# Optimization experiments

Hardware: AMD Instinct MI355X
Metric: run time of the kernel (lower is better)

## Reference

```python
import jax, jax.numpy as jnp
import numpy as np

C = 256; HEADS = 8; LEVELS = 4; POINTS = 4; D = C // HEADS
SPATIAL = np.array([[96, 96], [48, 48], [24, 24], [12, 12]], dtype=np.int32)  # (H, W) per level
AREAS = SPATIAL[:, 0] * SPATIAL[:, 1]
HW = int(AREAS.sum())  # 12240
LSI = np.concatenate([[0], np.cumsum(AREAS)[:-1]]).astype(np.int32)
N = 1; Q = HW


def setup_inputs() -> dict:
    key = jax.random.key(0)
    ks = jax.random.split(key, 12)
    s = 0.02
    return {
        "query": jax.random.normal(ks[0], (N, Q, C), jnp.float32),
        "reference_points": jax.random.uniform(ks[1], (N, Q, LEVELS, 2), jnp.float32),
        "input_flatten": jax.random.normal(ks[2], (N, HW, C), jnp.float32),
        "input_spatial_shapes": jnp.asarray(SPATIAL),
        "input_level_start_index": jnp.asarray(LSI),
        "W_off": jax.random.normal(ks[3], (C, HEADS * LEVELS * POINTS * 2), jnp.float32) * s,
        "b_off": jax.random.normal(ks[4], (HEADS * LEVELS * POINTS * 2,), jnp.float32) * s,
        "W_attn": jax.random.normal(ks[5], (C, HEADS * LEVELS * POINTS), jnp.float32) * s,
        "b_attn": jax.random.normal(ks[6], (HEADS * LEVELS * POINTS,), jnp.float32) * s,
        "W_val": jax.random.normal(ks[7], (C, C), jnp.float32) * (1.0 / np.sqrt(C)),
        "b_val": jax.random.normal(ks[8], (C,), jnp.float32) * s,
        "W_out": jax.random.normal(ks[9], (C, C), jnp.float32) * (1.0 / np.sqrt(C)),
        "b_out": jax.random.normal(ks[10], (C,), jnp.float32) * s,
    }


def _ms_deform_attn(query, reference_points, input_flatten, sp, lsi,
                    W_off, b_off, W_attn, b_attn, W_val, b_val, W_out, b_out):
    n, q, c = query.shape
    hw = input_flatten.shape[1]
    # value projection -> [N, Hd, HW, D]
    value = (input_flatten @ W_val + b_val).reshape(n, hw, HEADS, D).transpose(0, 2, 1, 3)
    # sampling offsets [N,Q,Hd,L,P,2]
    off = (query @ W_off + b_off).reshape(n, q, HEADS, LEVELS, POINTS, 2)
    # attention weights softmaxed over L*P (done inside the fused CUDA kernel)
    attn = jax.nn.softmax((query @ W_attn + b_attn).reshape(n, q, HEADS, LEVELS * POINTS), axis=-1)
    attn = attn.reshape(n, q, HEADS, LEVELS, POINTS)
    # normalized sampling locations (reference_points last dim == 2 branch)
    norm = jnp.stack([sp[:, 1], sp[:, 0]], -1).astype(query.dtype)  # (W, H) per level
    loc = reference_points[:, :, None, :, None, :] + off / norm[None, None, None, :, None, :]
    Hl = sp[:, 0][None, None, None, :, None]
    Wl = sp[:, 1][None, None, None, :, None]
    start = lsi[None, None, None, :, None]
    # grid_sample-style (align_corners=False) pixel coordinates
    x = loc[..., 0] * Wl - 0.5
    y = loc[..., 1] * Hl - 0.5
    x0 = jnp.floor(x); y0 = jnp.floor(y)
    lx = x - x0; ly = y - y0
    x0i = x0.astype(jnp.int32); y0i = y0.astype(jnp.int32)

    def gather(yi, xi):
        valid = (xi >= 0) & (xi < Wl) & (yi >= 0) & (yi < Hl)
        idx = jnp.where(valid, start + yi * Wl + xi, 0)  # [N,Q,Hd,L,P]
        idx_t = idx.transpose(0, 2, 1, 3, 4).reshape(n, HEADS, q * LEVELS * POINTS, 1)
        g = jnp.take_along_axis(value, idx_t, axis=2)  # [N,Hd,Q*L*P,D]
        g = g.reshape(n, HEADS, q, LEVELS, POINTS, D)
        return g * valid.transpose(0, 2, 1, 3, 4)[..., None]

    def w(a):
        return a.transpose(0, 2, 1, 3, 4)[..., None]  # [N,Hd,Q,L,P,1]

    sampled = (gather(y0i, x0i) * w((1 - ly) * (1 - lx))
               + gather(y0i, x0i + 1) * w((1 - ly) * lx)
               + gather(y0i + 1, x0i) * w(ly * (1 - lx))
               + gather(y0i + 1, x0i + 1) * w(ly * lx))  # [N,Hd,Q,L,P,D]
    out = jnp.einsum('nhqlpd,nqhlp->nqhd', sampled, attn).reshape(n, q, c)
    return out @ W_out + b_out


def reference(query, reference_points, input_flatten, input_spatial_shapes, input_level_start_index,
              W_off, b_off, W_attn, b_attn, W_val, b_val, W_out, b_out):
    return _ms_deform_attn(query, reference_points, input_flatten,
                           input_spatial_shapes, input_level_start_index,
                           W_off, b_off, W_attn, b_attn, W_val, b_val, W_out, b_out)
```

## Files before the change

### kernel.cpp

```cpp
#include <hip/hip_runtime.h>

#define QTOT 12240
#define KD   256

typedef float f32x4 __attribute__((ext_vector_type(4)));
typedef short s16x8 __attribute__((ext_vector_type(8)));
typedef unsigned short ushort_t;

__device__ __forceinline__ unsigned short f2b(float x) {
    union { float f; unsigned u; } c; c.f = x;
    unsigned r = c.u + 0x7fffu + ((c.u >> 16) & 1u);
    return (unsigned short)(r >> 16);
}
__device__ __forceinline__ int a_off(int row, int kb) { return row * 512 + (kb ^ ((row & 7) << 4)); }
__device__ __forceinline__ int b_off(int n,   int kb) { return n * 128 + (kb ^ ((n & 7) << 4)); }

__global__ __launch_bounds__(256) void prep(
    const float* __restrict__ W_val, const float* __restrict__ W_off,
    const float* __restrict__ W_attn, const float* __restrict__ W_out,
    const float* __restrict__ b_off, const float* __restrict__ b_attn,
    ushort_t* __restrict__ WvT, ushort_t* __restrict__ WcT,
    ushort_t* __restrict__ WoT, float* __restrict__ bcomb)
{
    int id = blockIdx.x * 256 + threadIdx.x;
    if (id < 65536) { int n = id >> 8, k = id & 255; WvT[id] = f2b(W_val[k * 256 + n]); }
    else if (id < 163840) {
        int t = id - 65536; int n = t >> 8, k = t & 255;
        float v = (n < 256) ? W_off[k * 256 + n] : W_attn[k * 128 + (n - 256)];
        WcT[t] = f2b(v);
    } else if (id < 229376) {
        int t = id - 163840; int n = t >> 8, k = t & 255;
        WoT[t] = f2b(W_out[k * 256 + n]);
    } else if (id < 229760) {
        int t = id - 229376; bcomb[t] = (t < 256) ? b_off[t] : b_attn[t - 256];
    }
}

template<int NF>
__device__ __forceinline__ void stageB(const ushort_t* __restrict__ WT, int k0, char* Bs) {
    const int tid = threadIdx.x;
#pragma unroll
    for (int e = 0; e < NF * 2; ++e) {
        int u = e * 256 + tid;
        int n = u >> 3, j = u & 7, js = j ^ (n & 7);
        s16x8 v = *(const s16x8*)(WT + (size_t)n * KD + k0 + js * 8);
        *(s16x8*)(Bs + n * 128 + j * 16) = v;
    }
}

template<int NF>
__device__ __forceinline__ void mm_full(const ushort_t* __restrict__ WT,
                                        char* As, char* Bs, f32x4 (&acc)[2][NF])
{
    const int tid = threadIdx.x, lane = tid & 63, wc = tid >> 6;
    const int lr = lane & 15, g8 = (lane >> 4) * 8;
    for (int k0 = 0; k0 < KD; k0 += 64) {
        __syncthreads();
#pragma unroll
        for (int kk = 0; kk < 2; ++kk) {
            const int kbB = (kk * 32 + g8) * 2;
            const int kbA = (k0 + kk * 32 + g8) * 2;
            s16x8 af0 = *(const s16x8*)(As + a_off(lr, kbA));
            s16x8 af1 = *(const s16x8*)(As + a_off(16 + lr, kbA));
#pragma unroll
            for (int n = 0; n < NF; ++n) {
                s16x8 bf = *(const s16x8*)(Bs + b_off(wc * NF * 16 + n * 16 + lr, kbB));
                acc[0][n] = __builtin_amdgcn_mfma_f32_16x16x32_bf16(af0, bf, acc[0][n], 0, 0, 0);
                acc[1][n] = __builtin_amdgcn_mfma_f32_16x16x32_bf16(af1, bf, acc[1][n], 0, 0, 0);
            }
        }
        __syncthreads();
        if (k0 < 192) stageB<NF>(WT, k0 + 64, Bs);
    }
}

__global__ __launch_bounds__(256) void gemm1(
    const float* __restrict__ inflat, const float* __restrict__ query,
    const ushort_t* __restrict__ WvT, const ushort_t* __restrict__ WcT,
    const float* __restrict__ b_val, const float* __restrict__ bcomb,
    ushort_t* __restrict__ projb, ushort_t* __restrict__ offb,
    float* __restrict__ logitf)
{
    __shared__ char smem[16384 + 49152];
    char* As = smem; char* Bs = smem + 16384;
    const int b = blockIdx.x;
    const bool isval = b < 383;
    const int bm = (isval ? b : b - 383) * 32;
    const float* A = isval ? inflat : query;

    {
        const int row = threadIdx.x >> 3, c0 = (threadIdx.x & 7) * 32;
        const int grow = bm + row;
        float4 f[8];
        if (grow < QTOT) {
            const float4* s = (const float4*)(A + (size_t)grow * KD + c0);
#pragma unroll
            for (int i = 0; i < 8; ++i) f[i] = s[i];
        } else {
#pragma unroll
            for (int i = 0; i < 8; ++i) f[i] = make_float4(0.f, 0.f, 0.f, 0.f);
        }
#pragma unroll
        for (int i = 0; i < 4; ++i) {
            s16x8 v;
            v[0] = f2b(f[2*i].x);   v[1] = f2b(f[2*i].y);
            v[2] = f2b(f[2*i].z);   v[3] = f2b(f[2*i].w);
            v[4] = f2b(f[2*i+1].x); v[5] = f2b(f[2*i+1].y);
            v[6] = f2b(f[2*i+1].z); v[7] = f2b(f[2*i+1].w);
            *(s16x8*)(As + a_off(row, (c0 + i * 8) * 2)) = v;
        }
    }

    const int lane = threadIdx.x & 63, wc = threadIdx.x >> 6;
    const int lr = lane & 15, rg = (lane >> 4) * 4;

    if (isval) {
        f32x4 acc[2][4];
#pragma unroll
        for (int m = 0; m < 2; ++m)
#pragma unroll
            for (int n = 0; n < 4; ++n) acc[m][n] = (f32x4)0.f;
        stageB<4>(WvT, 0, Bs);
        mm_full<4>(WvT, As, Bs, acc);
#pragma unroll
        for (int n = 0; n < 4; ++n) {
            const int col = wc * 64 + n * 16 + lr;
            const float bb = b_val[col];
#pragma unroll
            for (int m = 0; m < 2; ++m)
#pragma unroll
                for (int rr = 0; rr < 4; ++rr) {
                    const int row = bm + m * 16 + rg + rr;
                    if (row < QTOT) projb[(size_t)row * 256 + col] = f2b(acc[m][n][rr] + bb);
                }
        }
    } else {
        f32x4 acc[2][6];
#pragma unroll
        for (int m = 0; m < 2; ++m)
#pragma unroll
            for (int n = 0; n < 6; ++n) acc[m][n] = (f32x4)0.f;
        stageB<6>(WcT, 0, Bs);
        mm_full<6>(WcT, As, Bs, acc);
#pragma unroll
        for (int n = 0; n < 6; ++n) {
            const int col = wc * 96 + n * 16 + lr;
            const float bb = bcomb[col];
#pragma unroll
            for (int m = 0; m < 2; ++m)
#pragma unroll
                for (int rr = 0; rr < 4; ++rr) {
                    const int row = bm + m * 16 + rg + rr;
                    if (row >= QTOT) continue;
                    const float v = acc[m][n][rr] + bb;
                    if (col < 256) offb[(size_t)row * 256 + col] = f2b(v);
                    else           logitf[(size_t)row * 128 + col - 256] = v;
                }
        }
    }
}

__global__ __launch_bounds__(256) void sample4(
    const float* __restrict__ rp, const ushort_t* __restrict__ offb,
    const float* __restrict__ logitf, const ushort_t* __restrict__ projb,
    const int* __restrict__ sp, const int* __restrict__ lsi,
    ushort_t* __restrict__ outpre)
{
    const int bid = blockIdx.x;
    const int qpair = (bid & 7) * 765 + (bid >> 3);
    const int tid = threadIdx.x;
    const int qi = tid >> 7;
    const int q = qpair * 2 + qi;

    __shared__ int   s_idx[256][4];
    __shared__ float s_w[256][4];

    {
        const int t = tid & 127;
        const int l = (t >> 2) & 3;
        float logit = logitf[(size_t)q * 128 + t];
        float mx = logit;
#pragma unroll
        for (int d = 1; d < 16; d <<= 1) mx = fmaxf(mx, __shfl_xor(mx, d));
        float e = __expf(logit - mx);
        float s = e;
#pragma unroll
        for (int d = 1; d < 16; d <<= 1) s += __shfl_xor(s, d);
        const float aw = e / s;

        const unsigned opk = *(const unsigned*)&offb[(size_t)q * 256 + t * 2];
        const float ox = __uint_as_float(opk << 16);
        const float oy = __uint_as_float(opk & 0xffff0000u);

        const int Hl = sp[l * 2], Wl = sp[l * 2 + 1], st = lsi[l];
        const float rx = rp[((size_t)q * 4 + l) * 2 + 0];
        const float ry = rp[((size_t)q * 4 + l) * 2 + 1];

        const float x = rx * (float)Wl + ox - 0.5f;
        const float y = ry * (float)Hl + oy - 0.5f;
        const float xf = floorf(x), yf = floorf(y);
        const int x0 = (int)xf, y0 = (int)yf;
        const float lx = x - xf, ly = y - yf;

        const bool vx0 = (x0 >= 0) && (x0 < Wl);
        const bool vx1 = (x0 + 1 >= 0) && (x0 + 1 < Wl);
        const bool vy0 = (y0 >= 0) && (y0 < Hl);
        const bool vy1 = (y0 + 1 >= 0) && (y0 + 1 < Hl);

        s_w[tid][0] = (vx0 && vy0) ? aw * (1.f - ly) * (1.f - lx) : 0.f;
        s_w[tid][1] = (vx1 && vy0) ? aw * (1.f - ly) * lx         : 0.f;
        s_w[tid][2] = (vx0 && vy1) ? aw * ly * (1.f - lx)         : 0.f;
        s_w[tid][3] = (vx1 && vy1) ? aw * ly * lx                 : 0.f;
        s_idx[tid][0] = (vx0 && vy0) ? (st + y0 * Wl + x0) * 512           : 0;
        s_idx[tid][1] = (vx1 && vy0) ? (st + y0 * Wl + x0 + 1) * 512       : 0;
        s_idx[tid][2] = (vx0 && vy1) ? (st + (y0 + 1) * Wl + x0) * 512     : 0;
        s_idx[tid][3] = (vx1 && vy1) ? (st + (y0 + 1) * Wl + x0 + 1) * 512 : 0;
    }
    __syncthreads();

    const int tt = tid & 127;
    const int h = tt >> 4, qtr = (tt >> 2) & 3, c8 = tt & 3;
    const char* basec = (const char*)projb + (h * 32 + c8 * 8) * 2;

    float a0 = 0, a1 = 0, a2 = 0, a3 = 0, a4 = 0, a5 = 0, a6 = 0, a7 = 0;
#pragma unroll
    for (int p = 0; p < 4; ++p) {
        const int slot = qi * 128 + h * 16 + qtr * 4 + p;
        const int4   id4 = *(const int4*)s_idx[slot];
        const float4 w4  = *(const float4*)s_w[slot];
#pragma unroll
        for (int c = 0; c < 4; ++c) {
            const int   id = (c == 0) ? id4.x : (c == 1) ? id4.y : (c == 2) ? id4.z : id4.w;
            const float w  = (c == 0) ? w4.x  : (c == 1) ? w4.y  : (c == 2) ? w4.z  : w4.w;
            const uint4 v = *(const uint4*)(basec + id);
            a0 += w * __uint_as_float(v.x << 16);
            a1 += w * __uint_as_float(v.x & 0xffff0000u);
            a2 += w * __uint_as_float(v.y << 16);
            a3 += w * __uint_as_float(v.y & 0xffff0000u);
            a4 += w * __uint_as_float(v.z << 16);
            a5 += w * __uint_as_float(v.z & 0xffff0000u);
            a6 += w * __uint_as_float(v.w << 16);
            a7 += w * __uint_as_float(v.w & 0xffff0000u);
        }
    }
    a0 += __shfl_xor(a0, 4); a1 += __shfl_xor(a1, 4);
    a2 += __shfl_xor(a2, 4); a3 += __shfl_xor(a3, 4);
    a4 += __shfl_xor(a4, 4); a5 += __shfl_xor(a5, 4);
    a6 += __shfl_xor(a6, 4); a7 += __shfl_xor(a7, 4);
    a0 += __shfl_xor(a0, 8); a1 += __shfl_xor(a1, 8);
    a2 += __shfl_xor(a2, 8); a3 += __shfl_xor(a3, 8);
    a4 += __shfl_xor(a4, 8); a5 += __shfl_xor(a5, 8);
    a6 += __shfl_xor(a6, 8); a7 += __shfl_xor(a7, 8);

    if (qtr == 0) {
        uint4 o;
        o.x = (unsigned)f2b(a0) | ((unsigned)f2b(a1) << 16);
        o.y = (unsigned)f2b(a2) | ((unsigned)f2b(a3) << 16);
        o.z = (unsigned)f2b(a4) | ((unsigned)f2b(a5) << 16);
        o.w = (unsigned)f2b(a6) | ((unsigned)f2b(a7) << 16);
        *(uint4*)&outpre[(size_t)q * 256 + h * 32 + c8 * 8] = o;
    }
}

__global__ __launch_bounds__(256) void gemm_o(
    const ushort_t* __restrict__ Ab, const ushort_t* __restrict__ WoT,
    const float* __restrict__ b_out, float* __restrict__ out)
{
    __shared__ char smem[8192 + 32768];
    char* As = smem; char* Bs = smem + 8192;
    const int bm = blockIdx.x * 16;

    {
        const int row = threadIdx.x >> 4, cu = (threadIdx.x & 15) * 16;
        const s16x8* s = (const s16x8*)(Ab + (size_t)(bm + row) * KD + cu);
        s16x8 v0 = s[0], v1 = s[1];
        *(s16x8*)(As + a_off(row, cu * 2))      = v0;
        *(s16x8*)(As + a_off(row, cu * 2 + 16)) = v1;
    }

    f32x4 acc[4];
#pragma unroll
    for (int n = 0; n < 4; ++n) acc[n] = (f32x4)0.f;
    stageB<4>(WoT, 0, Bs);

    const int tid = threadIdx.x, lane = tid & 63, wc = tid >> 6;
    const int lr = lane & 15, g8 = (lane >> 4) * 8;
    for (int k0 = 0; k0 < KD; k0 += 64) {
        __syncthreads();
#pragma unroll
        for (int kk = 0; kk < 2; ++kk) {
            const int kbB = (kk * 32 + g8) * 2;
            const int kbA = (k0 + kk * 32 + g8) * 2;
            s16x8 af = *(const s16x8*)(As + a_off(lr, kbA));
#pragma unroll
            for (int n = 0; n < 4; ++n) {
                s16x8 bf = *(const s16x8*)(Bs + b_off(wc * 64 + n * 16 + lr, kbB));
                acc[n] = __builtin_amdgcn_mfma_f32_16x16x32_bf16(af, bf, acc[n], 0, 0, 0);
            }
        }
        __syncthreads();
        if (k0 < 192) stageB<4>(WoT, k0 + 64, Bs);
    }

    const int rg = (lane >> 4) * 4;
#pragma unroll
    for (int n = 0; n < 4; ++n) {
        const int col = wc * 64 + n * 16 + lr;
        const float bb = b_out[col];
#pragma unroll
        for (int rr = 0; rr < 4; ++rr) {
            const int row = bm + rg + rr;
            out[(size_t)row * 256 + col] = acc[n][rr] + bb;
        }
    }
}

extern "C" void kernel_launch(void* const* d_in, const int* in_sizes, int n_in,
                              void* d_out, int out_size, void* d_ws, size_t ws_size,
                              hipStream_t stream) {
    const float* query  = (const float*)d_in[0];
    const float* rp     = (const float*)d_in[1];
    const float* inflat = (const float*)d_in[2];
    const int*   sp     = (const int*)d_in[3];
    const int*   lsi    = (const int*)d_in[4];
    const float* W_off  = (const float*)d_in[5];
    const float* b_off  = (const float*)d_in[6];
    const float* W_attn = (const float*)d_in[7];
    const float* b_attn = (const float*)d_in[8];
    const float* W_val  = (const float*)d_in[9];
    const float* b_val  = (const float*)d_in[10];
    const float* W_out  = (const float*)d_in[11];
    const float* b_out  = (const float*)d_in[12];
    float* out = (float*)d_out;

    char* ws = (char*)d_ws;
    ushort_t* projb  = (ushort_t*)ws; ws += (size_t)QTOT * 256 * 2;
    ushort_t* offb   = (ushort_t*)ws; ws += (size_t)QTOT * 256 * 2;
    float*    logitf = (float*)ws;    ws += (size_t)QTOT * 128 * 4;
    ushort_t* outpre = (ushort_t*)ws; ws += (size_t)QTOT * 256 * 2;
    ushort_t* WvT    = (ushort_t*)ws; ws += 65536 * 2;
    ushort_t* WcT    = (ushort_t*)ws; ws += 98304 * 2;
    ushort_t* WoT    = (ushort_t*)ws; ws += 65536 * 2;
    float*    bcomb  = (float*)ws;    ws += 384 * 4;

    dim3 blk(256);

    prep<<<dim3(898), blk, 0, stream>>>(W_val, W_off, W_attn, W_out, b_off, b_attn,
                                        WvT, WcT, WoT, bcomb);

    gemm1<<<dim3(766), blk, 0, stream>>>(inflat, query, WvT, WcT, b_val, bcomb,
                                         projb, offb, logitf);

    sample4<<<dim3(6120), blk, 0, stream>>>(rp, offb, logitf, projb, sp, lsi, outpre);

    gemm_o<<<dim3(765), blk, 0, stream>>>(outpre, WoT, b_out, out);
}
```

Measured before the change: 70.23 us.

## Retile projection GEMMs into 64x64 output tiles with full-K shared staging

Both GEMM kernels move from narrow row tiles (32 or 16 rows) covering every output column to 64x64 output tiles, with the full K=256 slab of A and B staged into LDS once and a single barrier. The grid is enlarged and block indices are swizzled across 8 groups so more blocks can run concurrently. The intent is to remove the per-K-chunk barrier and staging loop and to raise parallelism. The cost is that the fp32 A rows are reloaded and reconverted once per column tile, which adds A-side global traffic, and the larger LDS footprint per block may reduce occupancy.

```diff
diff --git a/kernel.cpp b/kernel.cpp
--- a/kernel.cpp
+++ b/kernel.cpp
@@ -12,8 +12,7 @@
     unsigned r = c.u + 0x7fffu + ((c.u >> 16) & 1u);
     return (unsigned short)(r >> 16);
 }
-__device__ __forceinline__ int a_off(int row, int kb) { return row * 512 + (kb ^ ((row & 7) << 4)); }
-__device__ __forceinline__ int b_off(int n,   int kb) { return n * 128 + (kb ^ ((n & 7) << 4)); }
+__device__ __forceinline__ int swz(int row, int kb) { return row * 512 + (kb ^ ((row & 7) << 4)); }
 
 __global__ __launch_bounds__(256) void prep(
     const float* __restrict__ W_val, const float* __restrict__ W_off,
@@ -36,41 +35,30 @@
     }
 }
 
-template<int NF>
-__device__ __forceinline__ void stageB(const ushort_t* __restrict__ WT, int k0, char* Bs) {
-    const int tid = threadIdx.x;
-#pragma unroll
-    for (int e = 0; e < NF * 2; ++e) {
-        int u = e * 256 + tid;
-        int n = u >> 3, j = u & 7, js = j ^ (n & 7);
-        s16x8 v = *(const s16x8*)(WT + (size_t)n * KD + k0 + js * 8);
-        *(s16x8*)(Bs + n * 128 + j * 16) = v;
-    }
-}
-
-template<int NF>
-__device__ __forceinline__ void mm_full(const ushort_t* __restrict__ WT,
-                                        char* As, char* Bs, f32x4 (&acc)[2][NF])
-{
-    const int tid = threadIdx.x, lane = tid & 63, wc = tid >> 6;
+__device__ __forceinline__ void stageB_full(const ushort_t* __restrict__ WT, int bn, char* Bs) {
+    const int t = threadIdx.x;
+    const int n = t >> 2, c0 = (t & 3) * 64;
+    const ushort_t* src = WT + (size_t)(bn + n) * KD + c0;
+#pragma unroll
+    for (int j = 0; j < 8; ++j)
+        *(s16x8*)(Bs + swz(n, (c0 + j * 8) * 2)) = *(const s16x8*)(src + j * 8);
+}
+
+__device__ __forceinline__ void mm64(char* As, char* Bs, f32x4 (&acc)[2][2]) {
+    const int tid = threadIdx.x, lane = tid & 63, wave = tid >> 6;
+    const int wr = wave >> 1, wc = wave & 1;
     const int lr = lane & 15, g8 = (lane >> 4) * 8;
-    for (int k0 = 0; k0 < KD; k0 += 64) {
-        __syncthreads();
-#pragma unroll
-        for (int kk = 0; kk < 2; ++kk) {
-            const int kbB = (kk * 32 + g8) * 2;
-            const int kbA = (k0 + kk * 32 + g8) * 2;
-            s16x8 af0 = *(const s16x8*)(As + a_off(lr, kbA));
-            s16x8 af1 = *(const s16x8*)(As + a_off(16 + lr, kbA));
-#pragma unroll
-            for (int n = 0; n < NF; ++n) {
-                s16x8 bf = *(const s16x8*)(Bs + b_off(wc * NF * 16 + n * 16 + lr, kbB));
-                acc[0][n] = __builtin_amdgcn_mfma_f32_16x16x32_bf16(af0, bf, acc[0][n], 0, 0, 0);
-                acc[1][n] = __builtin_amdgcn_mfma_f32_16x16x32_bf16(af1, bf, acc[1][n], 0, 0, 0);
-            }
-        }
-        __syncthreads();
-        if (k0 < 192) stageB<NF>(WT, k0 + 64, Bs);
+#pragma unroll
+    for (int kc = 0; kc < 8; ++kc) {
+        const int kb = (kc * 32 + g8) * 2;
+        s16x8 a0 = *(const s16x8*)(As + swz(wr * 32 + lr,      kb));
+        s16x8 a1 = *(const s16x8*)(As + swz(wr * 32 + 16 + lr, kb));
+        s16x8 b0 = *(const s16x8*)(Bs + swz(wc * 32 + lr,      kb));
+        s16x8 b1 = *(const s16x8*)(Bs + swz(wc * 32 + 16 + lr, kb));
+        acc[0][0] = __builtin_amdgcn_mfma_f32_16x16x32_bf16(a0, b0, acc[0][0], 0, 0, 0);
+        acc[0][1] = __builtin_amdgcn_mfma_f32_16x16x32_bf16(a0, b1, acc[0][1], 0, 0, 0);
+        acc[1][0] = __builtin_amdgcn_mfma_f32_16x16x32_bf16(a1, b0, acc[1][0], 0, 0, 0);
+        acc[1][1] = __builtin_amdgcn_mfma_f32_16x16x32_bf16(a1, b1, acc[1][1], 0, 0, 0);
     }
 }
 
@@ -81,82 +69,124 @@
     ushort_t* __restrict__ projb, ushort_t* __restrict__ offb,
     float* __restrict__ logitf)
 {
-    __shared__ char smem[16384 + 49152];
-    char* As = smem; char* Bs = smem + 16384;
-    const int b = blockIdx.x;
-    const bool isval = b < 383;
-    const int bm = (isval ? b : b - 383) * 32;
-    const float* A = isval ? inflat : query;
+    __shared__ char As[32768];
+    __shared__ char Bs[32768];
+    const int bid = blockIdx.x;
+    const int linear = (bid & 7) * 240 + (bid >> 3);
+    const int mt = linear / 10, nt = linear - mt * 10;
+    const int bm = mt * 64;
+    const bool isval = nt < 4;
+    const int bnc = isval ? nt * 64 : (nt - 4) * 64;
+
+    if (isval) stageB_full(WvT, bnc, Bs);
+    else       stageB_full(WcT, bnc, Bs);
 
     {
-        const int row = threadIdx.x >> 3, c0 = (threadIdx.x & 7) * 32;
+        const int t = threadIdx.x;
+        const int row = t >> 2, c0 = (t & 3) * 64;
         const int grow = bm + row;
-        float4 f[8];
+        const float* A = isval ? inflat : query;
+        float4 f[16];
         if (grow < QTOT) {
             const float4* s = (const float4*)(A + (size_t)grow * KD + c0);
 #pragma unroll
-            for (int i = 0; i < 8; ++i) f[i] = s[i];
+            for (int i = 0; i < 16; ++i) f[i] = s[i];
         } else {
 #pragma unroll
-            for (int i = 0; i < 8; ++i) f[i] = make_float4(0.f, 0.f, 0.f, 0.f);
+            for (int i = 0; i < 16; ++i) f[i] = make_float4(0.f, 0.f, 0.f, 0.f);
         }
 #pragma unroll
-        for (int i = 0; i < 4; ++i) {
+        for (int j = 0; j < 8; ++j) {
             s16x8 v;
-            v[0] = f2b(f[2*i].x);   v[1] = f2b(f[2*i].y);
-            v[2] = f2b(f[2*i].z);   v[3] = f2b(f[2*i].w);
-            v[4] = f2b(f[2*i+1].x); v[5] = f2b(f[2*i+1].y);
-            v[6] = f2b(f[2*i+1].z); v[7] = f2b(f[2*i+1].w);
-            *(s16x8*)(As + a_off(row, (c0 + i * 8) * 2)) = v;
+            v[0] = f2b(f[2*j].x);   v[1] = f2b(f[2*j].y);
+            v[2] = f2b(f[2*j].z);   v[3] = f2b(f[2*j].w);
+            v[4] = f2b(f[2*j+1].x); v[5] = f2b(f[2*j+1].y);
+            v[6] = f2b(f[2*j+1].z); v[7] = f2b(f[2*j+1].w);
+            *(s16x8*)(As + swz(row, (c0 + j * 8) * 2)) = v;
         }
     }
-
-    const int lane = threadIdx.x & 63, wc = threadIdx.x >> 6;
+    __syncthreads();
+
+    f32x4 acc[2][2];
+#pragma unroll
+    for (int m = 0; m < 2; ++m)
+#pragma unroll
+        for (int n = 0; n < 2; ++n) acc[m][n] = (f32x4)0.f;
+    mm64(As, Bs, acc);
+
+    const int lane = threadIdx.x & 63, wave = threadIdx.x >> 6;
+    const int wr = wave >> 1, wc = wave & 1;
     const int lr = lane & 15, rg = (lane >> 4) * 4;
-
-    if (isval) {
-        f32x4 acc[2][4];
+#pragma unroll
+    for (int n = 0; n < 2; ++n) {
+        const int col = bnc + wc * 32 + n * 16 + lr;
+        const float bb = isval ? b_val[col] : bcomb[col];
 #pragma unroll
         for (int m = 0; m < 2; ++m)
 #pragma unroll
-            for (int n = 0; n < 4; ++n) acc[m][n] = (f32x4)0.f;
-        stageB<4>(WvT, 0, Bs);
-        mm_full<4>(WvT, As, Bs, acc);
-#pragma unroll
-        for (int n = 0; n < 4; ++n) {
-            const int col = wc * 64 + n * 16 + lr;
-            const float bb = b_val[col];
-#pragma unroll
-            for (int m = 0; m < 2; ++m)
-#pragma unroll
-                for (int rr = 0; rr < 4; ++rr) {
-                    const int row = bm + m * 16 + rg + rr;
-                    if (row < QTOT) projb[(size_t)row * 256 + col] = f2b(acc[m][n][rr] + bb);
-                }
+            for (int rr = 0; rr < 4; ++rr) {
+                const int row = bm + wr * 32 + m * 16 + rg + rr;
+                if (row >= QTOT) continue;
+                const float v = acc[m][n][rr] + bb;
+                if (isval)          projb[(size_t)row * 256 + col] = f2b(v);
+                else if (col < 256) offb [(size_t)row * 256 + col] = f2b(v);
+                else                logitf[(size_t)row * 128 + col - 256] = v;
+            }
+    }
+}
+
+__global__ __launch_bounds__(256) void gemm_o(
+    const ushort_t* __restrict__ Ab, const ushort_t* __restrict__ WoT,
+    const float* __restrict__ b_out, float* __restrict__ out)
+{
+    __shared__ char As[32768];
+    __shared__ char Bs[32768];
+    const int bid = blockIdx.x;
+    const int linear = (bid & 7) * 96 + (bid >> 3);
+    const int mt = linear >> 2, nt = linear & 3;
+    const int bm = mt * 64;
+
+    stageB_full(WoT, nt * 64, Bs);
+
+    {
+        const int t = threadIdx.x;
+        const int row = t >> 2, c0 = (t & 3) * 64;
+        const int grow = bm + row;
+        if (grow < QTOT) {
+            const ushort_t* s = Ab + (size_t)grow * KD + c0;
+#pragma unroll
+            for (int j = 0; j < 8; ++j)
+                *(s16x8*)(As + swz(row, (c0 + j * 8) * 2)) = *(const s16x8*)(s + j * 8);
+        } else {
+            s16x8 z = (s16x8)0;
+#pragma unroll
+            for (int j = 0; j < 8; ++j)
+                *(s16x8*)(As + swz(row, (c0 + j * 8) * 2)) = z;
         }
-    } else {
-        f32x4 acc[2][6];
+    }
+    __syncthreads();
+
+    f32x4 acc[2][2];
+#pragma unroll
+    for (int m = 0; m < 2; ++m)
+#pragma unroll
+        for (int n = 0; n < 2; ++n) acc[m][n] = (f32x4)0.f;
+    mm64(As, Bs, acc);
+
+    const int lane = threadIdx.x & 63, wave = threadIdx.x >> 6;
+    const int wr = wave >> 1, wc = wave & 1;
+    const int lr = lane & 15, rg = (lane >> 4) * 4;
+#pragma unroll
+    for (int n = 0; n < 2; ++n) {
+        const int col = nt * 64 + wc * 32 + n * 16 + lr;
+        const float bb = b_out[col];
 #pragma unroll
         for (int m = 0; m < 2; ++m)
 #pragma unroll
-            for (int n = 0; n < 6; ++n) acc[m][n] = (f32x4)0.f;
-        stageB<6>(WcT, 0, Bs);
-        mm_full<6>(WcT, As, Bs, acc);
-#pragma unroll
-        for (int n = 0; n < 6; ++n) {
-            const int col = wc * 96 + n * 16 + lr;
-            const float bb = bcomb[col];
-#pragma unroll
-            for (int m = 0; m < 2; ++m)
-#pragma unroll
-                for (int rr = 0; rr < 4; ++rr) {
-                    const int row = bm + m * 16 + rg + rr;
-                    if (row >= QTOT) continue;
-                    const float v = acc[m][n][rr] + bb;
-                    if (col < 256) offb[(size_t)row * 256 + col] = f2b(v);
-                    else           logitf[(size_t)row * 128 + col - 256] = v;
-                }
-        }
+            for (int rr = 0; rr < 4; ++rr) {
+                const int row = bm + wr * 32 + m * 16 + rg + rr;
+                if (row < QTOT) out[(size_t)row * 256 + col] = acc[m][n][rr] + bb;
+            }
     }
 }
 
@@ -259,59 +289,6 @@
         o.z = (unsigned)f2b(a4) | ((unsigned)f2b(a5) << 16);
         o.w = (unsigned)f2b(a6) | ((unsigned)f2b(a7) << 16);
         *(uint4*)&outpre[(size_t)q * 256 + h * 32 + c8 * 8] = o;
-    }
-}
-
-__global__ __launch_bounds__(256) void gemm_o(
-    const ushort_t* __restrict__ Ab, const ushort_t* __restrict__ WoT,
-    const float* __restrict__ b_out, float* __restrict__ out)
-{
-    __shared__ char smem[8192 + 32768];
-    char* As = smem; char* Bs = smem + 8192;
-    const int bm = blockIdx.x * 16;
-
-    {
-        const int row = threadIdx.x >> 4, cu = (threadIdx.x & 15) * 16;
-        const s16x8* s = (const s16x8*)(Ab + (size_t)(bm + row) * KD + cu);
-        s16x8 v0 = s[0], v1 = s[1];
-        *(s16x8*)(As + a_off(row, cu * 2))      = v0;
-        *(s16x8*)(As + a_off(row, cu * 2 + 16)) = v1;
-    }
-
-    f32x4 acc[4];
-#pragma unroll
-    for (int n = 0; n < 4; ++n) acc[n] = (f32x4)0.f;
-    stageB<4>(WoT, 0, Bs);
-
-    const int tid = threadIdx.x, lane = tid & 63, wc = tid >> 6;
-    const int lr = lane & 15, g8 = (lane >> 4) * 8;
-    for (int k0 = 0; k0 < KD; k0 += 64) {
-        __syncthreads();
-#pragma unroll
-        for (int kk = 0; kk < 2; ++kk) {
-            const int kbB = (kk * 32 + g8) * 2;
-            const int kbA = (k0 + kk * 32 + g8) * 2;
-            s16x8 af = *(const s16x8*)(As + a_off(lr, kbA));
-#pragma unroll
-            for (int n = 0; n < 4; ++n) {
-                s16x8 bf = *(const s16x8*)(Bs + b_off(wc * 64 + n * 16 + lr, kbB));
-                acc[n] = __builtin_amdgcn_mfma_f32_16x16x32_bf16(af, bf, acc[n], 0, 0, 0);
-            }
-        }
-        __syncthreads();
-        if (k0 < 192) stageB<4>(WoT, k0 + 64, Bs);
-    }
-
-    const int rg = (lane >> 4) * 4;
-#pragma unroll
-    for (int n = 0; n < 4; ++n) {
-        const int col = wc * 64 + n * 16 + lr;
-        const float bb = b_out[col];
-#pragma unroll
-        for (int rr = 0; rr < 4; ++rr) {
-            const int row = bm + rg + rr;
-            out[(size_t)row * 256 + col] = acc[n][rr] + bb;
-        }
     }
 }
 
@@ -348,10 +325,10 @@
     prep<<<dim3(898), blk, 0, stream>>>(W_val, W_off, W_attn, W_out, b_off, b_attn,
                                         WvT, WcT, WoT, bcomb);
 
-    gemm1<<<dim3(766), blk, 0, stream>>>(inflat, query, WvT, WcT, b_val, bcomb,
-                                         projb, offb, logitf);
+    gemm1<<<dim3(1920), blk, 0, stream>>>(inflat, query, WvT, WcT, b_val, bcomb,
+                                          projb, offb, logitf);
 
     sample4<<<dim3(6120), blk, 0, stream>>>(rp, offb, logitf, projb, sp, lsi, outpre);
 
-    gemm_o<<<dim3(765), blk, 0, stream>>>(outpre, WoT, b_out, out);
-}
+    gemm_o<<<dim3(768), blk, 0, stream>>>(outpre, WoT, b_out, out);
+}
```

After: 82.77 us. 17.9% more time.
